# Kernel tuning notes

Hardware: AMD Instinct MI355X
Metric: run time of the kernel (lower is better)

The kernel has to match this reference:

```python
import jax, jax.numpy as jnp
import numpy as np

B, H, W, C = 8, 56, 56, 256
HEADS = 8      # block-level heads; each branch uses HEADS//2
SPLIT = 7      # split_size
EPS = 1e-5


def _ln(x, g, b):
    m = x.mean(-1, keepdims=True)
    v = ((x - m) ** 2).mean(-1, keepdims=True)
    return (x - m) * jax.lax.rsqrt(v + EPS) * g + b


def _lepe_attn(q, k, v, H_sp, W_sp, heads, cw, cb):
    # q,k,v: [B,H,W,Ch]; cross-shaped window attention with LePE depthwise conv bias
    Bq, Hq, Wq, Ch = q.shape
    hd = Ch // heads
    scale = hd ** -0.5
    nh, nw = Hq // H_sp, Wq // W_sp

    def win(t):  # -> [Bw, heads, L, hd]  (Bw = B*nh*nw, L = H_sp*W_sp)
        t = t.reshape(Bq, nh, H_sp, nw, W_sp, Ch).transpose(0, 1, 3, 2, 4, 5)
        return t.reshape(-1, H_sp * W_sp, heads, hd).transpose(0, 2, 1, 3)

    qw, kw = win(q), win(k)
    # v windows laid out NCHW for the depthwise LePE conv
    vimg = v.reshape(Bq, nh, H_sp, nw, W_sp, Ch).transpose(0, 1, 3, 5, 2, 4).reshape(-1, Ch, H_sp, W_sp)
    lepe = jax.lax.conv_general_dilated(
        vimg, cw, window_strides=(1, 1), padding=((1, 1), (1, 1)),
        feature_group_count=Ch, dimension_numbers=("NCHW", "OIHW", "NCHW"))
    lepe = lepe + cb[None, :, None, None]
    lepe = lepe.reshape(-1, heads, hd, H_sp * W_sp).transpose(0, 1, 3, 2)
    vw = vimg.reshape(-1, heads, hd, H_sp * W_sp).transpose(0, 1, 3, 2)

    attn = jax.nn.softmax(jnp.einsum("whld,whmd->whlm", qw * scale, kw), axis=-1)
    out = jnp.einsum("whlm,whmd->whld", attn, vw) + lepe  # [Bw,heads,L,hd]
    out = out.transpose(0, 2, 1, 3).reshape(-1, H_sp, W_sp, Ch)
    # windows2img
    out = out.reshape(Bq, nh, nw, H_sp, W_sp, Ch).transpose(0, 1, 3, 2, 4, 5).reshape(Bq, Hq, Wq, Ch)
    return out


def setup_inputs() -> dict:
    key = jax.random.key(0)
    ks = jax.random.split(key, 8)
    ch = C // 2
    s = 0.02
    return {
        "x": jax.random.normal(ks[0], (B, H, W, C), jnp.float32),
        "gamma1": jnp.ones((C,), jnp.float32), "beta1": jnp.zeros((C,), jnp.float32),
        "w_qkv": jax.random.normal(ks[1], (C, 3 * C), jnp.float32) * s,
        "lepe_w0": jax.random.normal(ks[2], (ch, 1, 3, 3), jnp.float32) * s,
        "lepe_b0": jnp.zeros((ch,), jnp.float32),
        "lepe_w1": jax.random.normal(ks[3], (ch, 1, 3, 3), jnp.float32) * s,
        "lepe_b1": jnp.zeros((ch,), jnp.float32),
        "w_proj": jax.random.normal(ks[4], (C, C), jnp.float32) * s,
        "b_proj": jnp.zeros((C,), jnp.float32),
        "gamma2": jnp.ones((C,), jnp.float32), "beta2": jnp.zeros((C,), jnp.float32),
        "w_fc1": jax.random.normal(ks[5], (C, 4 * C), jnp.float32) * s,
        "b_fc1": jnp.zeros((4 * C,), jnp.float32),
        "w_fc2": jax.random.normal(ks[6], (4 * C, C), jnp.float32) * s,
        "b_fc2": jnp.zeros((C,), jnp.float32),
    }


def reference(x, gamma1, beta1, w_qkv, lepe_w0, lepe_b0, lepe_w1, lepe_b1,
              w_proj, b_proj, gamma2, beta2, w_fc1, b_fc1, w_fc2, b_fc2):
    Bx, Hx, Wx, Cx = x.shape
    img = _ln(x, gamma1, beta1)
    qkv = (img @ w_qkv).reshape(Bx, Hx, Wx, 3, Cx).transpose(3, 0, 1, 2, 4)
    q, k, v = qkv[0], qkv[1], qkv[2]
    ch = Cx // 2
    heads = HEADS // 2
    # branch 0 (idx=0): H_sp=H, W_sp=split  -> vertical stripes
    x0 = _lepe_attn(q[..., :ch], k[..., :ch], v[..., :ch], Hx, SPLIT, heads, lepe_w0, lepe_b0)
    # branch 1 (idx=1): H_sp=split, W_sp=W  -> horizontal stripes
    x1 = _lepe_attn(q[..., ch:], k[..., ch:], v[..., ch:], SPLIT, Wx, heads, lepe_w1, lepe_b1)
    att = jnp.concatenate([x0, x1], axis=-1) @ w_proj + b_proj
    x = x + att
    h = _ln(x, gamma2, beta2)
    h = jax.nn.gelu(h @ w_fc1 + b_fc1, approximate=False) @ w_fc2 + b_fc2
    return x + h
```

## Files before the change

kernel.cpp:

```cpp
#include <hip/hip_runtime.h>
#include <stdint.h>

typedef __attribute__((ext_vector_type(4))) float  f32x4;
typedef __attribute__((ext_vector_type(8))) __bf16 bf16x8;

#define DEVI static __device__ __forceinline__

DEVI float bf2f_lo(uint32_t u) { union { uint32_t i; float f; } v; v.i = u << 16;          return v.f; }
DEVI float bf2f_hi(uint32_t u) { union { uint32_t i; float f; } v; v.i = u & 0xffff0000u;  return v.f; }
DEVI uint16_t f2bf(float f) {
    union { float f; uint32_t i; } v; v.f = f;
    uint32_t r = v.i + 0x7fffu + ((v.i >> 16) & 1u);
    return (uint16_t)(r >> 16);
}
DEVI void unpack8(uint4 u, float* f) {
    f[0] = bf2f_lo(u.x); f[1] = bf2f_hi(u.x);
    f[2] = bf2f_lo(u.y); f[3] = bf2f_hi(u.y);
    f[4] = bf2f_lo(u.z); f[5] = bf2f_hi(u.z);
    f[6] = bf2f_lo(u.w); f[7] = bf2f_hi(u.w);
}
DEVI void gload_lds16(const uint16_t* gp, uint16_t* lp) {
    __builtin_amdgcn_global_load_lds(
        (const __attribute__((address_space(1))) uint32_t*)gp,
        (__attribute__((address_space(3))) uint32_t*)lp, 16, 0, 0);
}

__global__ __launch_bounds__(256) void wprep(const float* __restrict__ w,
                                             uint16_t* __restrict__ wt, int K, int N) {
    int idx = blockIdx.x * 256 + threadIdx.x;
    if (idx >= K * N) return;
    int k = idx / N, n = idx - k * N;
    wt[(size_t)n * K + k] = f2bf(w[idx]);
}

__global__ __launch_bounds__(256) void ln_kernel(const float* __restrict__ x,
                                                 const float* __restrict__ g,
                                                 const float* __restrict__ be,
                                                 uint16_t* __restrict__ y) {
    int row  = blockIdx.x * 4 + (threadIdx.x >> 6);
    int lane = threadIdx.x & 63;
    const float* xr = x + (size_t)row * 256 + lane * 4;
    f32x4 v = *(const f32x4*)xr;
    float s  = v[0] + v[1] + v[2] + v[3];
    float s2 = v[0]*v[0] + v[1]*v[1] + v[2]*v[2] + v[3]*v[3];
#pragma unroll
    for (int off = 32; off > 0; off >>= 1) {
        s  += __shfl_xor(s, off);
        s2 += __shfl_xor(s2, off);
    }
    float mean = s * (1.f / 256.f);
    float var  = s2 * (1.f / 256.f) - mean * mean;
    float rs   = rsqrtf(var + 1e-5f);
    f32x4 gv = *(const f32x4*)(g  + lane * 4);
    f32x4 bv = *(const f32x4*)(be + lane * 4);
    uint64_t pk = 0;
#pragma unroll
    for (int j = 0; j < 4; ++j) {
        uint64_t b = f2bf((v[j] - mean) * rs * gv[j] + bv[j]);
        pk |= b << (16 * j);
    }
    *(uint64_t*)(y + (size_t)row * 256 + lane * 4) = pk;
}

template <int EPI>
__global__ __launch_bounds__(256) void gemm_bt(const uint16_t* __restrict__ A,
                                               const uint16_t* __restrict__ Bt,
                                               int M, int N, int K,
                                               const float* __restrict__ bias,
                                               const float* __restrict__ resid,
                                               void* __restrict__ outp) {
    __shared__ __align__(16) uint16_t As[2][128 * 32];
    __shared__ __align__(16) uint16_t Bs[2][128 * 32];
    const int tid  = threadIdx.x;
    const int lane = tid & 63;
    const int w    = tid >> 6;
    const int wr   = w >> 1, wc = w & 1;
    const int bm = blockIdx.x, bn = blockIdx.y;
    f32x4 acc[4][4] = {};
    const int nk = K >> 5;
    const int wb = w * 512;

    const int srow = tid >> 2;
    const int hwr  = (srow ^ (srow >> 2)) & 3;
    const size_t ao0 = (size_t)srow * K + (size_t)(((tid & 3) ^ hwr) * 8);
    const size_t ao1 = ao0 + (size_t)64 * K;

    const uint16_t* Abase = A  + (size_t)bm * 128 * K;
    const uint16_t* Bbase = Bt + (size_t)bn * 128 * K;

    auto stage = [&](int buf, int kk) {
        const uint16_t* Ab = Abase + kk * 32;
        const uint16_t* Bb = Bbase + kk * 32;
        gload_lds16(Ab + ao0, &As[buf][wb]);
        gload_lds16(Ab + ao1, &As[buf][wb + 2048]);
        gload_lds16(Bb + ao0, &Bs[buf][wb]);
        gload_lds16(Bb + ao1, &Bs[buf][wb + 2048]);
    };

    stage(0, 0);
    __syncthreads();
    int cur = 0;

    const int li = lane & 15;
    const int rA = wr * 64 + li;
    const int rB = wc * 64 + li;
    const int kx = ((lane >> 4) ^ ((li ^ (li >> 2)) & 3)) * 8;

    for (int kk = 0; kk < nk; ++kk) {
        if (kk + 1 < nk) stage(cur ^ 1, kk + 1);

        bf16x8 af[4], bfr[4];
#pragma unroll
        for (int m = 0; m < 4; ++m)
            af[m] = __builtin_bit_cast(bf16x8,
                     *(const uint4*)&As[cur][(rA + m * 16) * 32 + kx]);
#pragma unroll
        for (int n = 0; n < 4; ++n)
            bfr[n] = __builtin_bit_cast(bf16x8,
                      *(const uint4*)&Bs[cur][(rB + n * 16) * 32 + kx]);
#pragma unroll
        for (int m = 0; m < 4; ++m)
#pragma unroll
            for (int n = 0; n < 4; ++n)
                acc[m][n] = __builtin_amdgcn_mfma_f32_16x16x32_bf16(af[m], bfr[n], acc[m][n], 0, 0, 0);

        __syncthreads();
        cur ^= 1;
    }

    const int row0 = bm * 128 + wr * 64 + ((lane >> 4) * 4);
    const int col0 = bn * 128 + wc * 64 + li;
#pragma unroll
    for (int m = 0; m < 4; ++m) {
#pragma unroll
        for (int n = 0; n < 4; ++n) {
            const int col = col0 + n * 16;
#pragma unroll
            for (int r = 0; r < 4; ++r) {
                const int row = row0 + m * 16 + r;
                float v = acc[m][n][r];
                size_t idx = (size_t)row * N + col;
                if (EPI == 0) {
                    ((uint16_t*)outp)[idx] = f2bf(v);
                } else if (EPI == 1) {
                    ((float*)outp)[idx] = v + bias[col] + resid[idx];
                } else {
                    v += bias[col];
                    float ge = 0.5f * v * (1.0f + erff(v * 0.70710678118654752f));
                    ((uint16_t*)outp)[idx] = f2bf(ge);
                }
            }
        }
    }
}

__global__ __launch_bounds__(64) void attn_mfma(const uint16_t* __restrict__ qkv,
                                                uint16_t* __restrict__ att) {
    __shared__ __align__(16) uint16_t Pl[32 * 40];
    int bid = ((int)blockIdx.x & 7) * 832 + ((int)blockIdx.x >> 3);
    const int sub   = bid % 52;
    const int winl  = bid / 52;
    const int qtile = sub % 13;
    const int head  = sub / 13;
    const int win   = winl & 63;
    const int branch = winl >> 6;
    const int lane = threadIdx.x;
    const int g  = lane >> 4;
    const int li = lane & 15;
    const int b = win >> 3, wp = win & 7;
    const int ch0 = branch * 128 + head * 32;
    const int base0 = b * 3136;
    const int woff  = wp * 7;
    const int toks1 = base0 + wp * 392;

    auto tokof = [&](int l) -> int {
        if (branch == 0) { int r = l / 7; return base0 + r * 56 + woff + (l - r * 7); }
        return toks1 + l;
    };
    const int tok391 = tokof(391);
    const int q0 = qtile * 32;

    bf16x8 qf[2];
#pragma unroll
    for (int nb = 0; nb < 2; ++nb) {
        int ql = q0 + nb * 16 + li; if (ql > 391) ql = 391;
        qf[nb] = __builtin_bit_cast(bf16x8,
                 *(const uint4*)(qkv + (size_t)tokof(ql) * 768 + ch0 + g * 8));
    }

    float m_run[2], s_run[2];
    f32x4 oacc[2][2];
#pragma unroll
    for (int nb = 0; nb < 2; ++nb) {
        m_run[nb] = -1e30f; s_run[nb] = 0.f;
        oacc[0][nb] = (f32x4)0.f; oacc[1][nb] = (f32x4)0.f;
    }
    const float c = 0.25503486f;
    const float THR = 31.368f;

    for (int kt = 0; kt < 13; ++kt) {
        const int kbase = kt * 32;
        bf16x8 kf[2];
#pragma unroll
        for (int mb = 0; mb < 2; ++mb) {
            int kl = kbase + mb * 16 + li; if (kl > 391) kl = 391;
            kf[mb] = __builtin_bit_cast(bf16x8,
                     *(const uint4*)(qkv + (size_t)tokof(kl) * 768 + 256 + ch0 + g * 8));
        }
        uint16_t vg0[8], vg1[8];
        {
            int kl0 = kbase + g * 8;
            int tk, cc = 0;
            if (branch == 0) { int r = kl0 / 7; cc = kl0 - r * 7; tk = base0 + r * 56 + woff + cc; }
            else tk = toks1 + kl0;
#pragma unroll
            for (int j = 0; j < 8; ++j) {
                int t = (kl0 + j > 391) ? tok391 : tk;
                const uint16_t* vp = qkv + (size_t)t * 768 + 512 + ch0 + li;
                vg0[j] = vp[0];
                vg1[j] = vp[16];
                if (branch == 0) { if (++cc == 7) { cc = 0; tk += 50; } else ++tk; }
                else ++tk;
            }
        }
        f32x4 sa[2][2] = {};
#pragma unroll
        for (int mb = 0; mb < 2; ++mb)
#pragma unroll
            for (int nb = 0; nb < 2; ++nb)
                sa[mb][nb] = __builtin_amdgcn_mfma_f32_16x16x32_bf16(kf[mb], qf[nb], sa[mb][nb], 0, 0, 0);
        if (kt == 12) {
#pragma unroll
            for (int nb = 0; nb < 2; ++nb)
#pragma unroll
                for (int r = 0; r < 4; ++r) {
                    if (g >= 2) sa[0][nb][r] = -1e30f;
                    sa[1][nb][r] = -1e30f;
                }
        }
#pragma unroll
        for (int nb = 0; nb < 2; ++nb) {
            float mt = fmaxf(fmaxf(fmaxf(sa[0][nb][0], sa[0][nb][1]), fmaxf(sa[0][nb][2], sa[0][nb][3])),
                             fmaxf(fmaxf(sa[1][nb][0], sa[1][nb][1]), fmaxf(sa[1][nb][2], sa[1][nb][3])));
            mt = fmaxf(mt, __shfl_xor(mt, 16));
            mt = fmaxf(mt, __shfl_xor(mt, 32));
            if (!__all(mt <= m_run[nb] + THR)) {
                float m_new = fmaxf(m_run[nb], mt);
                float corr = exp2f((m_run[nb] - m_new) * c);
                m_run[nb] = m_new;
                s_run[nb] *= corr;
#pragma unroll
                for (int mb = 0; mb < 2; ++mb)
#pragma unroll
                    for (int r = 0; r < 4; ++r) oacc[mb][nb][r] *= corr;
            }
            const float m2 = m_run[nb] * c;
            float psum = 0.f;
            uint32_t pk[4];
#pragma unroll
            for (int mb = 0; mb < 2; ++mb) {
                float p0 = exp2f(fmaf(sa[mb][nb][0], c, -m2));
                float p1 = exp2f(fmaf(sa[mb][nb][1], c, -m2));
                float p2 = exp2f(fmaf(sa[mb][nb][2], c, -m2));
                float p3 = exp2f(fmaf(sa[mb][nb][3], c, -m2));
                psum += (p0 + p1) + (p2 + p3);
                union { __bf16 h[2]; uint32_t u; } ca, cb;
                ca.h[0] = (__bf16)p0; ca.h[1] = (__bf16)p1;
                cb.h[0] = (__bf16)p2; cb.h[1] = (__bf16)p3;
                pk[mb * 2 + 0] = ca.u;
                pk[mb * 2 + 1] = cb.u;
            }
            psum += __shfl_xor(psum, 16);
            psum += __shfl_xor(psum, 32);
            s_run[nb] += psum;
            uint32_t* dst = (uint32_t*)&Pl[(li + 16 * nb) * 40];
            dst[g * 2 + 0] = pk[0];
            dst[g * 2 + 1] = pk[1];
            dst[g * 2 + 8] = pk[2];
            dst[g * 2 + 9] = pk[3];
        }
        union { uint16_t u[8]; bf16x8 v; } cv0, cv1;
#pragma unroll
        for (int j = 0; j < 8; ++j) { cv0.u[j] = vg0[j]; cv1.u[j] = vg1[j]; }
        bf16x8 vf0 = cv0.v, vf1 = cv1.v;
        bf16x8 pf[2];
#pragma unroll
        for (int nb = 0; nb < 2; ++nb)
            pf[nb] = __builtin_bit_cast(bf16x8,
                     *(const uint4*)&Pl[(li + 16 * nb) * 40 + g * 8]);
#pragma unroll
        for (int nb = 0; nb < 2; ++nb) {
            oacc[0][nb] = __builtin_amdgcn_mfma_f32_16x16x32_bf16(vf0, pf[nb], oacc[0][nb], 0, 0, 0);
            oacc[1][nb] = __builtin_amdgcn_mfma_f32_16x16x32_bf16(vf1, pf[nb], oacc[1][nb], 0, 0, 0);
        }
    }
#pragma unroll
    for (int nb = 0; nb < 2; ++nb) {
        int ql = q0 + nb * 16 + li;
        if (ql <= 391) {
            float rn = 1.f / s_run[nb];
            uint16_t* op = att + (size_t)tokof(ql) * 256 + ch0;
#pragma unroll
            for (int mb = 0; mb < 2; ++mb)
#pragma unroll
                for (int r = 0; r < 4; ++r)
                    op[mb * 16 + g * 4 + r] = f2bf(oacc[mb][nb][r] * rn);
        }
    }
}

__global__ __launch_bounds__(256) void lepe_kernel(const uint16_t* __restrict__ qkv,
                                                   const float* __restrict__ lw0,
                                                   const float* __restrict__ lb0,
                                                   const float* __restrict__ lw1,
                                                   const float* __restrict__ lb1,
                                                   uint16_t* __restrict__ att) {
    __shared__ float wl[9][256];
    __shared__ float bl[256];
    {
        int tid = threadIdx.x;
        for (int i = tid; i < 2304; i += 256) {
            int tap = i >> 8, ch = i & 255;
            wl[tap][ch] = (ch < 128) ? lw0[ch * 9 + tap] : lw1[(ch - 128) * 9 + tap];
        }
        bl[tid] = (tid < 128) ? lb0[tid] : lb1[tid - 128];
    }
    __syncthreads();

    int idx = blockIdx.x * 256 + threadIdx.x;
    int t = idx >> 5, cg = idx & 31;
    int ch = cg * 8;
    int branch = ch >> 7;
    int b = t / 3136, rem = t - b * 3136, h = rem / 56, w = rem - h * 56;
    int r0, r1, c0, c1;
    if (branch == 0) { r0 = 0; r1 = 55; int wp = w / 7; c0 = wp * 7; c1 = c0 + 6; }
    else             { int hp = h / 7; r0 = hp * 7; r1 = r0 + 6; c0 = 0; c1 = 55; }

    const uint16_t* vbase = qkv + (size_t)b * 3136 * 768 + 512 + ch;
    float acc[8];
    {
        f32x4 b0 = *(const f32x4*)&bl[ch];
        f32x4 b1 = *(const f32x4*)&bl[ch + 4];
#pragma unroll
        for (int d = 0; d < 4; ++d) { acc[d] = b0[d]; acc[d + 4] = b1[d]; }
    }
#pragma unroll
    for (int dy = -1; dy <= 1; ++dy) {
#pragma unroll
        for (int dx = -1; dx <= 1; ++dx) {
            int hh = h + dy, ww = w + dx;
            float mask = (hh >= r0 && hh <= r1 && ww >= c0 && ww <= c1) ? 1.f : 0.f;
            int hc = min(max(hh, r0), r1), wc = min(max(ww, c0), c1);
            uint4 u = *(const uint4*)(vbase + (size_t)(hc * 56 + wc) * 768);
            float vv[8]; unpack8(u, vv);
            const int tap = (dy + 1) * 3 + (dx + 1);
            f32x4 w0 = *(const f32x4*)&wl[tap][ch];
            f32x4 w1 = *(const f32x4*)&wl[tap][ch + 4];
#pragma unroll
            for (int d = 0; d < 4; ++d) {
                acc[d]     += (mask * w0[d]) * vv[d];
                acc[d + 4] += (mask * w1[d]) * vv[d + 4];
            }
        }
    }
    uint16_t* ap = att + (size_t)t * 256 + ch;
    uint4 a = *(const uint4*)ap;
    float av[8]; unpack8(a, av);
    uint16_t ob[8];
#pragma unroll
    for (int d = 0; d < 8; ++d) ob[d] = f2bf(av[d] + acc[d]);
    *(uint4*)ap = *(const uint4*)ob;
}

extern "C" void kernel_launch(void* const* d_in, const int* in_sizes, int n_in,
                              void* d_out, int out_size, void* d_ws, size_t ws_size,
                              hipStream_t stream) {
    const float* x      = (const float*)d_in[0];
    const float* g1     = (const float*)d_in[1];
    const float* be1    = (const float*)d_in[2];
    const float* w_qkv  = (const float*)d_in[3];
    const float* lw0    = (const float*)d_in[4];
    const float* lb0    = (const float*)d_in[5];
    const float* lw1    = (const float*)d_in[6];
    const float* lb1    = (const float*)d_in[7];
    const float* w_proj = (const float*)d_in[8];
    const float* b_proj = (const float*)d_in[9];
    const float* g2     = (const float*)d_in[10];
    const float* be2    = (const float*)d_in[11];
    const float* w_fc1  = (const float*)d_in[12];
    const float* b_fc1  = (const float*)d_in[13];
    const float* w_fc2  = (const float*)d_in[14];
    const float* b_fc2  = (const float*)d_in[15];
    float* out = (float*)d_out;

    char* p = (char*)d_ws;
    auto carve = [&](size_t bytes) -> char* {
        char* q = p; p += (bytes + 255) & ~(size_t)255; return q;
    };
    uint16_t* lnb    = (uint16_t*)carve((size_t)25088 * 256 * 2);
    uint16_t* qkvh   = (uint16_t*)carve((size_t)25088 * 1024 * 2);
    uint16_t* attb   = (uint16_t*)carve((size_t)25088 * 256 * 2);
    float*    x1     = (float*)   carve((size_t)25088 * 256 * 4);
    uint16_t* wqkvT  = (uint16_t*)carve((size_t)768 * 256 * 2);
    uint16_t* wprojT = (uint16_t*)carve((size_t)256 * 256 * 2);
    uint16_t* wfc1T  = (uint16_t*)carve((size_t)1024 * 256 * 2);
    uint16_t* wfc2T  = (uint16_t*)carve((size_t)256 * 1024 * 2);

    wprep<<<768,  256, 0, stream>>>(w_qkv,  wqkvT,  256, 768);
    wprep<<<256,  256, 0, stream>>>(w_proj, wprojT, 256, 256);
    wprep<<<1024, 256, 0, stream>>>(w_fc1,  wfc1T,  256, 1024);
    wprep<<<1024, 256, 0, stream>>>(w_fc2,  wfc2T,  1024, 256);

    ln_kernel<<<6272, 256, 0, stream>>>(x, g1, be1, lnb);
    gemm_bt<0><<<dim3(196, 6), 256, 0, stream>>>(lnb, wqkvT, 25088, 768, 256,
                                                 nullptr, nullptr, qkvh);
    attn_mfma<<<6656, 64, 0, stream>>>(qkvh, attb);
    lepe_kernel<<<3136, 256, 0, stream>>>(qkvh, lw0, lb0, lw1, lb1, attb);
    gemm_bt<1><<<dim3(196, 2), 256, 0, stream>>>(attb, wprojT, 25088, 256, 256,
                                                 b_proj, x, x1);
    ln_kernel<<<6272, 256, 0, stream>>>(x1, g2, be2, lnb);
    gemm_bt<2><<<dim3(196, 8), 256, 0, stream>>>(lnb, wfc1T, 25088, 1024, 256,
                                                 b_fc1, nullptr, qkvh);
    gemm_bt<1><<<dim3(196, 2), 256, 0, stream>>>(qkvh, wfc2T, 25088, 256, 1024,
                                                 b_fc2, x1, out);
}
```

Baseline: 300.6 us.

## Stage V tiles in double-buffered LDS with transpose reads; merge weight prep launches

The attention kernel used to gather V with 16 scalar 2-byte global loads per lane per key tile. It now loads V with 16-byte vector loads into a double-buffered LDS tile, prefetching the next tile during the current iteration, and builds the MFMA operands with ds_read_b64_tr_b16 transpose reads. This targets the cost of uncoalesced narrow global loads, in exchange for extra LDS traffic, an explicit lgkmcnt wait, and a scheduling barrier. Separately, the four weight-conversion launches are merged into one to cut launch overhead.

```diff
diff --git a/kernel.cpp b/kernel.cpp
--- a/kernel.cpp
+++ b/kernel.cpp
@@ -3,6 +3,7 @@
 
 typedef __attribute__((ext_vector_type(4))) float  f32x4;
 typedef __attribute__((ext_vector_type(8))) __bf16 bf16x8;
+typedef __attribute__((address_space(3))) uint16_t lds_u16;
 
 #define DEVI static __device__ __forceinline__
 
@@ -24,13 +25,28 @@
         (const __attribute__((address_space(1))) uint32_t*)gp,
         (__attribute__((address_space(3))) uint32_t*)lp, 16, 0, 0);
 }
-
-__global__ __launch_bounds__(256) void wprep(const float* __restrict__ w,
-                                             uint16_t* __restrict__ wt, int K, int N) {
+DEVI uint2 trr(const lds_u16* a) {
+    uint2 d;
+    asm volatile("ds_read_b64_tr_b16 %0, %1" : "=v"(d) : "v"(a) : "memory");
+    return d;
+}
+
+__global__ __launch_bounds__(256) void wprep4(const float* __restrict__ w_qkv,
+                                              const float* __restrict__ w_proj,
+                                              const float* __restrict__ w_fc1,
+                                              const float* __restrict__ w_fc2,
+                                              uint16_t* __restrict__ dqkv,
+                                              uint16_t* __restrict__ dproj,
+                                              uint16_t* __restrict__ dfc1,
+                                              uint16_t* __restrict__ dfc2) {
     int idx = blockIdx.x * 256 + threadIdx.x;
-    if (idx >= K * N) return;
+    const float* w; uint16_t* d; int K, N;
+    if (idx < 196608)      { w = w_qkv;  d = dqkv;  K = 256;  N = 768;  }
+    else if (idx < 262144) { w = w_proj; d = dproj; K = 256;  N = 256;  idx -= 196608; }
+    else if (idx < 524288) { w = w_fc1;  d = dfc1;  K = 256;  N = 1024; idx -= 262144; }
+    else                   { w = w_fc2;  d = dfc2;  K = 1024; N = 256;  idx -= 524288; }
     int k = idx / N, n = idx - k * N;
-    wt[(size_t)n * K + k] = f2bf(w[idx]);
+    d[(size_t)n * K + k] = f2bf(w[idx]);
 }
 
 __global__ __launch_bounds__(256) void ln_kernel(const float* __restrict__ x,
@@ -157,6 +173,7 @@
 __global__ __launch_bounds__(64) void attn_mfma(const uint16_t* __restrict__ qkv,
                                                 uint16_t* __restrict__ att) {
     __shared__ __align__(16) uint16_t Pl[32 * 40];
+    __shared__ __align__(16) uint16_t Vb[2][2][32][16];
     int bid = ((int)blockIdx.x & 7) * 832 + ((int)blockIdx.x >> 3);
     const int sub   = bid % 52;
     const int winl  = bid / 52;
@@ -177,8 +194,11 @@
         if (branch == 0) { int r = l / 7; return base0 + r * 56 + woff + (l - r * 7); }
         return toks1 + l;
     };
-    const int tok391 = tokof(391);
+    auto vtok = [&](int key) -> int { return tokof(key > 391 ? 391 : key); };
     const int q0 = qtile * 32;
+
+    const int skey = lane >> 1;
+    const int sch  = (lane & 1) * 8;
 
     bf16x8 qf[2];
 #pragma unroll
@@ -198,6 +218,15 @@
     const float c = 0.25503486f;
     const float THR = 31.368f;
 
+    {
+        const uint16_t* vp = qkv + (size_t)vtok(skey) * 768 + 512 + ch0 + sch;
+        uint4 ra = *(const uint4*)vp;
+        uint4 rb = *(const uint4*)(vp + 16);
+        *(uint4*)&Vb[0][0][skey][sch] = ra;
+        *(uint4*)&Vb[0][1][skey][sch] = rb;
+    }
+    int cur = 0;
+
     for (int kt = 0; kt < 13; ++kt) {
         const int kbase = kt * 32;
         bf16x8 kf[2];
@@ -207,21 +236,12 @@
             kf[mb] = __builtin_bit_cast(bf16x8,
                      *(const uint4*)(qkv + (size_t)tokof(kl) * 768 + 256 + ch0 + g * 8));
         }
-        uint16_t vg0[8], vg1[8];
-        {
-            int kl0 = kbase + g * 8;
-            int tk, cc = 0;
-            if (branch == 0) { int r = kl0 / 7; cc = kl0 - r * 7; tk = base0 + r * 56 + woff + cc; }
-            else tk = toks1 + kl0;
-#pragma unroll
-            for (int j = 0; j < 8; ++j) {
-                int t = (kl0 + j > 391) ? tok391 : tk;
-                const uint16_t* vp = qkv + (size_t)t * 768 + 512 + ch0 + li;
-                vg0[j] = vp[0];
-                vg1[j] = vp[16];
-                if (branch == 0) { if (++cc == 7) { cc = 0; tk += 50; } else ++tk; }
-                else ++tk;
-            }
+        uint4 ra, rb;
+        const bool more = (kt + 1 < 13);
+        if (more) {
+            const uint16_t* vp = qkv + (size_t)vtok(kbase + 32 + skey) * 768 + 512 + ch0 + sch;
+            ra = *(const uint4*)vp;
+            rb = *(const uint4*)(vp + 16);
         }
         f32x4 sa[2][2] = {};
 #pragma unroll
@@ -279,10 +299,21 @@
             dst[g * 2 + 8] = pk[2];
             dst[g * 2 + 9] = pk[3];
         }
-        union { uint16_t u[8]; bf16x8 v; } cv0, cv1;
-#pragma unroll
-        for (int j = 0; j < 8; ++j) { cv0.u[j] = vg0[j]; cv1.u[j] = vg1[j]; }
-        bf16x8 vf0 = cv0.v, vf1 = cv1.v;
+        if (more) {
+            *(uint4*)&Vb[cur ^ 1][0][skey][sch] = ra;
+            *(uint4*)&Vb[cur ^ 1][1][skey][sch] = rb;
+        }
+        const lds_u16* vb = (const lds_u16*)&Vb[cur][0][0][0];
+        const lds_u16* p0 = vb + g * 128 + li;
+        uint2 t0 = trr(p0);
+        uint2 t1 = trr(p0 + 64);
+        uint2 t2 = trr(p0 + 512);
+        uint2 t3 = trr(p0 + 512 + 64);
+        asm volatile("s_waitcnt lgkmcnt(0)" ::: "memory");
+        __builtin_amdgcn_sched_barrier(0);
+        bf16x8 vf0 = __builtin_bit_cast(bf16x8, uint4{t0.x, t0.y, t1.x, t1.y});
+        bf16x8 vf1 = __builtin_bit_cast(bf16x8, uint4{t2.x, t2.y, t3.x, t3.y});
+
         bf16x8 pf[2];
 #pragma unroll
         for (int nb = 0; nb < 2; ++nb)
@@ -293,6 +324,7 @@
             oacc[0][nb] = __builtin_amdgcn_mfma_f32_16x16x32_bf16(vf0, pf[nb], oacc[0][nb], 0, 0, 0);
             oacc[1][nb] = __builtin_amdgcn_mfma_f32_16x16x32_bf16(vf1, pf[nb], oacc[1][nb], 0, 0, 0);
         }
+        cur ^= 1;
     }
 #pragma unroll
     for (int nb = 0; nb < 2; ++nb) {
@@ -406,10 +438,8 @@
     uint16_t* wfc1T  = (uint16_t*)carve((size_t)1024 * 256 * 2);
     uint16_t* wfc2T  = (uint16_t*)carve((size_t)256 * 1024 * 2);
 
-    wprep<<<768,  256, 0, stream>>>(w_qkv,  wqkvT,  256, 768);
-    wprep<<<256,  256, 0, stream>>>(w_proj, wprojT, 256, 256);
-    wprep<<<1024, 256, 0, stream>>>(w_fc1,  wfc1T,  256, 1024);
-    wprep<<<1024, 256, 0, stream>>>(w_fc2,  wfc2T,  1024, 256);
+    wprep4<<<3072, 256, 0, stream>>>(w_qkv, w_proj, w_fc1, w_fc2,
+                                     wqkvT, wprojT, wfc1T, wfc2T);
 
     ln_kernel<<<6272, 256, 0, stream>>>(x, g1, be1, lnb);
     gemm_bt<0><<<dim3(196, 6), 256, 0, stream>>>(lnb, wqkvT, 25088, 768, 256,
```

Result: faster. 290.3 us (-3.5%).
